# Kernel tuning notes

Measured on AMD Instinct MI355X. Metric: run time of the kernel, lower is better.

The kernel has to match this reference:

```python
import jax, jax.numpy as jnp
import numpy as np

N = 100000   # nodes
E = 1600000  # edges per meta-path graph
D_IN = 256
H = 4        # num_heads
F = 32       # out_feats per head
D_HID = H * F  # 128
D_SEM = 128  # semantic attention hidden dim
C = 8        # output classes
NEG_SLOPE = 0.2


def setup_inputs() -> dict:
    key = jax.random.key(0)
    ks = jax.random.split(key, 24)
    inp = {
        "x": jax.random.normal(ks[0], (N, D_IN), dtype=jnp.float32),
        "src0": jax.random.randint(ks[1], (E,), 0, N),
        "dst0": jax.random.randint(ks[2], (E,), 0, N),
        "ew0": jax.random.uniform(ks[3], (E,), dtype=jnp.float32),
        "src1": jax.random.randint(ks[4], (E,), 0, N),
        "dst1": jax.random.randint(ks[5], (E,), 0, N),
        "ew1": jax.random.uniform(ks[6], (E,), dtype=jnp.float32),
    }
    s_in = 1.0 / np.sqrt(D_IN)
    s_f = 1.0 / np.sqrt(F)
    s_h = 1.0 / np.sqrt(D_HID)
    s_s = 1.0 / np.sqrt(D_SEM)
    # GAT params for meta-path 0 and 1 (tuple feat -> separate fc_src/fc_dst)
    inp["Wsrc0"] = jax.random.normal(ks[7], (D_IN, D_HID), dtype=jnp.float32) * s_in
    inp["Wdst0"] = jax.random.normal(ks[8], (D_IN, D_HID), dtype=jnp.float32) * s_in
    inp["al0"] = jax.random.normal(ks[9], (H, F), dtype=jnp.float32) * s_f
    inp["ar0"] = jax.random.normal(ks[10], (H, F), dtype=jnp.float32) * s_f
    inp["b0"] = jnp.zeros((D_HID,), dtype=jnp.float32)
    inp["Wsrc1"] = jax.random.normal(ks[11], (D_IN, D_HID), dtype=jnp.float32) * s_in
    inp["Wdst1"] = jax.random.normal(ks[12], (D_IN, D_HID), dtype=jnp.float32) * s_in
    inp["al1"] = jax.random.normal(ks[13], (H, F), dtype=jnp.float32) * s_f
    inp["ar1"] = jax.random.normal(ks[14], (H, F), dtype=jnp.float32) * s_f
    inp["b1"] = jnp.zeros((D_HID,), dtype=jnp.float32)
    # Semantic attention: Linear(D_HID->128) -> tanh -> Linear(128->1, no bias)
    inp["Wp1"] = jax.random.normal(ks[15], (D_HID, D_SEM), dtype=jnp.float32) * s_h
    inp["bp1"] = jnp.zeros((D_SEM,), dtype=jnp.float32)
    inp["Wp2"] = jax.random.normal(ks[16], (D_SEM, 1), dtype=jnp.float32) * s_s
    # Prediction head
    inp["Wo"] = jax.random.normal(ks[17], (D_HID, C), dtype=jnp.float32) * s_h
    inp["bo"] = jnp.zeros((C,), dtype=jnp.float32)
    return inp


def gat_conv(x, Wsrc, Wdst, al, ar, b, src, dst, ew):
    # feat_src/feat_dst: [N, H, F]
    fs = (x @ Wsrc).reshape(N, H, F)
    fd = (x @ Wdst).reshape(N, H, F)
    el = jnp.einsum('nhf,hf->nh', fs, al)  # [N, H]
    er = jnp.einsum('nhf,hf->nh', fd, ar)  # [N, H]
    e = jax.nn.leaky_relu(el[src] + er[dst], negative_slope=NEG_SLOPE)  # [E, H]
    a = jax.nn.sigmoid(e) * ew[:, None]  # [E, H]  (sigmoid attention * edge_weight)
    m = fs[src] * a[:, :, None]  # [E, H, F]
    out = jax.ops.segment_sum(m, dst, num_segments=N)  # [N, H, F]
    out = out + b.reshape(1, H, F)
    return jax.nn.elu(out).reshape(N, H * F)


def semantic_attention(z, Wp1, bp1, Wp2):
    # z: [N, P, D_HID]
    w = jnp.tanh(z @ Wp1 + bp1) @ Wp2  # [N, P, 1]
    w = w.mean(axis=0)                  # [P, 1]
    beta = jax.nn.softmax(w, axis=0)    # softmax over meta-paths
    return (beta[None] * z).sum(axis=1)  # [N, D_HID]


def reference(x, src0, dst0, ew0, src1, dst1, ew1,
              Wsrc0, Wdst0, al0, ar0, b0,
              Wsrc1, Wdst1, al1, ar1, b1,
              Wp1, bp1, Wp2, Wo, bo):
    z0 = gat_conv(x, Wsrc0, Wdst0, al0, ar0, b0, src0, dst0, ew0)
    z1 = gat_conv(x, Wsrc1, Wdst1, al1, ar1, b1, src1, dst1, ew1)
    z = jnp.stack([z0, z1], axis=1)  # [N, 2, H*F]
    h = semantic_attention(z, Wp1, bp1, Wp2)  # [N, H*F]
    return h @ Wo + bo  # [N, C]
```

## Files before the change

### kernel.cpp

```cpp
#include <hip/hip_runtime.h>
#include <hip/hip_fp16.h>
#include <math.h>

#define N_NODES 100000
#define N_EDGES 1600000
#define D_IN    256
#define D_HID   128
#define NH      4
#define NF      32
#define D_SEM   128
#define NC      8
#define NEG_SLOPE 0.2f
#define BUCKET  64
#define BIN_SHIFT 9
#define BINS    196
#define BIN_CAP 9216
#define CHUNK   8192

typedef _Float16 half8 __attribute__((ext_vector_type(8)));
typedef float    floatx4 __attribute__((ext_vector_type(4)));

__global__ void prep_fold(const float* __restrict__ Ws0, const float* __restrict__ al0,
                          const float* __restrict__ Wd0, const float* __restrict__ ar0,
                          const float* __restrict__ Ws1, const float* __restrict__ al1,
                          const float* __restrict__ Wd1, const float* __restrict__ ar1,
                          float* __restrict__ WF) {
    int d = threadIdx.x;
    for (int p = 0; p < 2; ++p) {
        const float* Ws = p ? Ws1 : Ws0;
        const float* al = p ? al1 : al0;
        const float* Wd = p ? Wd1 : Wd0;
        const float* ar = p ? ar1 : ar0;
        for (int h = 0; h < NH; ++h) {
            float se = 0.f, sr = 0.f;
            for (int f = 0; f < NF; ++f) {
                se = fmaf(Ws[d*D_HID + h*NF + f], al[h*NF + f], se);
                sr = fmaf(Wd[d*D_HID + h*NF + f], ar[h*NF + f], sr);
            }
            WF[d*16 + p*8 + h]     = se;
            WF[d*16 + p*8 + 4 + h] = sr;
        }
    }
}

__global__ __launch_bounds__(256) void prep_tr(const float* __restrict__ Ws0,
                                               const float* __restrict__ Ws1,
                                               const float* __restrict__ Wp1,
                                               __half* __restrict__ WT0,
                                               __half* __restrict__ WT1,
                                               __half* __restrict__ WP1T) {
    int g = blockIdx.x * 256 + threadIdx.x;
    if (g < 32768) {
        int c = g >> 8, k = g & 255;
        WT0[g] = __float2half_rn(Ws0[k*D_HID + c]);
    } else if (g < 65536) {
        int g2 = g - 32768;
        int c = g2 >> 8, k = g2 & 255;
        WT1[g2] = __float2half_rn(Ws1[k*D_HID + c]);
    } else {
        int g2 = g - 65536;
        int c = g2 >> 7, k = g2 & 127;
        WP1T[g2] = __float2half_rn(Wp1[k*D_SEM + c]);
    }
}

__global__ __launch_bounds__(256) void er_el_kernel(const float* __restrict__ x,
                                                    const float* __restrict__ WF,
                                                    float* __restrict__ eler,
                                                    __half* __restrict__ XH) {
    __shared__ float xs[16][260];
    __shared__ float wfs[4096];
    int tid = threadIdx.x;
    #pragma unroll
    for (int i = 0; i < 16; ++i) wfs[tid + i*256] = WF[tid + i*256];
    int n0 = blockIdx.x * 16;
    #pragma unroll
    for (int i = 0; i < 4; ++i) {
        int id = tid + i*256;
        int r = id >> 6, c = (id & 63) << 2;
        *(float4*)&xs[r][c] = *(const float4*)&x[(size_t)(n0 + r)*D_IN + c];
    }
    __syncthreads();
    int node = tid >> 4, c = tid & 15;
    float s = 0.f;
    #pragma unroll 8
    for (int k = 0; k < 256; ++k) s = fmaf(xs[node][k], wfs[k*16 + c], s);
    int p = c >> 3, e = (c >> 2) & 1, h = c & 3;
    eler[(p*2 + e)*400000 + (n0 + node)*4 + h] = s;

    #pragma unroll
    for (int i = 0; i < 4; ++i) {
        int id = tid + i*256;
        int r = id >> 6, c4 = (id & 63) << 2;
        float4 v = *(const float4*)&xs[r][c4];
        __half2 h0 = __floats2half2_rn(v.x, v.y);
        __half2 h1 = __floats2half2_rn(v.z, v.w);
        uint2 pk; pk.x = *(unsigned*)&h0; pk.y = *(unsigned*)&h1;
        *(uint2*)&XH[(size_t)(n0 + r)*D_IN + c4] = pk;
    }
}

__global__ __launch_bounds__(256) void gemm_fs_mfma(const __half* __restrict__ XH,
                                                    const __half* __restrict__ WT,
                                                    __half* __restrict__ FS) {
    __shared__ unsigned short xs[64][64];
    __shared__ unsigned short ws[128][64];
    int tid = threadIdx.x;
    int row0 = blockIdx.x * 64;
    int wid = tid >> 6, lane = tid & 63;
    int wm = wid >> 1, wn = wid & 1;
    int lr = lane & 15, lk = lane >> 4;

    floatx4 acc[2][4];
    #pragma unroll
    for (int m = 0; m < 2; ++m)
        #pragma unroll
        for (int n = 0; n < 4; ++n) acc[m][n] = (floatx4){0.f, 0.f, 0.f, 0.f};

    for (int k0 = 0; k0 < D_IN; k0 += 64) {
        #pragma unroll
        for (int i = 0; i < 2; ++i) {
            int id = tid + i*256;
            int r = id >> 3, c8 = (id & 7) << 3;
            int grow = row0 + r;
            uint4 pk = make_uint4(0u, 0u, 0u, 0u);
            if (grow < N_NODES) pk = *(const uint4*)&XH[(size_t)grow*D_IN + k0 + c8];
            int cc = (((c8 >> 3) ^ (r & 7)) << 3);
            *(uint4*)&xs[r][cc] = pk;
        }
        #pragma unroll
        for (int i = 0; i < 8; ++i) {
            int id = tid + i*256;
            int col = id >> 4, c4 = (id & 15) << 2;
            uint2 pk = *(const uint2*)&WT[col*256 + k0 + c4];
            int cc = (((c4 >> 3) ^ (col & 7)) << 3) + (c4 & 7);
            *(uint2*)&ws[col][cc] = pk;
        }
        __syncthreads();
        #pragma unroll
        for (int kk = 0; kk < 2; ++kk) {
            int ksub = kk*4 + lk;
            half8 a[2], b[4];
            #pragma unroll
            for (int m = 0; m < 2; ++m) {
                int r = wm*32 + m*16 + lr;
                a[m] = *(half8*)&xs[r][((ksub ^ (r & 7)) << 3)];
            }
            #pragma unroll
            for (int n = 0; n < 4; ++n) {
                int c = wn*64 + n*16 + lr;
                b[n] = *(half8*)&ws[c][((ksub ^ (c & 7)) << 3)];
            }
            #pragma unroll
            for (int m = 0; m < 2; ++m)
                #pragma unroll
                for (int n = 0; n < 4; ++n)
                    acc[m][n] = __builtin_amdgcn_mfma_f32_16x16x32_f16(a[m], b[n], acc[m][n], 0, 0, 0);
        }
        __syncthreads();
    }

    unsigned short* outs = &ws[0][0];
    #pragma unroll
    for (int m = 0; m < 2; ++m)
        #pragma unroll
        for (int n = 0; n < 4; ++n) {
            int col = wn*64 + n*16 + lr;
            #pragma unroll
            for (int r4 = 0; r4 < 4; ++r4) {
                int rr = wm*32 + m*16 + lk*4 + r4;
                __half hv = __float2half_rn(acc[m][n][r4]);
                outs[rr*128 + col] = *(unsigned short*)&hv;
            }
        }
    __syncthreads();
    #pragma unroll
    for (int i = 0; i < 8; ++i) {
        int id = tid + i*256;
        int r = id >> 5, c4 = (id & 31) << 2;
        int grow = row0 + r;
        if (grow < N_NODES)
            *(uint2*)&FS[(size_t)grow*D_HID + c4] = *(uint2*)&outs[r*128 + c4];
    }
}

__global__ __launch_bounds__(1024) void bin_kernel(const int* __restrict__ src,
                                                   const int* __restrict__ dst,
                                                   const float* __restrict__ ew,
                                                   int* __restrict__ gcur,
                                                   uint2* __restrict__ binned) {
    __shared__ uint2 stage[CHUNK];
    __shared__ unsigned char binof[CHUNK];
    __shared__ int bcnt[256], boff[256], gbase[256], brun[256];
    int tid = threadIdx.x;
    int c0 = blockIdx.x * CHUNK;
    int C = N_EDGES - c0; if (C > CHUNK) C = CHUNK;
    if (C <= 0) return;

    if (tid < 256) bcnt[tid] = 0;
    __syncthreads();
    for (int j = tid; j < C; j += 1024)
        atomicAdd(&bcnt[dst[c0 + j] >> BIN_SHIFT], 1);
    __syncthreads();

    int v = (tid < 256) ? bcnt[tid] : 0;
    if (tid < 256) boff[tid] = v;
    __syncthreads();
    for (int o = 1; o < 256; o <<= 1) {
        int u = (tid < 256 && tid >= o) ? boff[tid - o] : 0;
        __syncthreads();
        if (tid < 256) boff[tid] += u;
        __syncthreads();
    }
    if (tid < 256) {
        boff[tid] -= v;
        brun[tid] = 0;
        if (tid < BINS) gbase[tid] = v ? atomicAdd(&gcur[tid], v) : 0;
    }
    __syncthreads();

    for (int j = tid; j < C; j += 1024) {
        int e = c0 + j;
        int d = dst[e];
        int b = d >> BIN_SHIFT;
        unsigned q = (unsigned)(ew[e] * 32767.f + 0.5f);
        int p = atomicAdd(&brun[b], 1);
        int sl = boff[b] + p;
        stage[sl] = make_uint2(((unsigned)src[e] << 15) | q, (unsigned)d);
        binof[sl] = (unsigned char)b;
    }
    __syncthreads();

    for (int j = tid; j < C; j += 1024) {
        int b = binof[j];
        int off = gbase[b] + (j - boff[b]);
        if (off < BIN_CAP) binned[b * BIN_CAP + off] = stage[j];
    }
}

__global__ __launch_bounds__(1024) void bucket_kernel(const int* __restrict__ gcur,
                                                      const uint2* __restrict__ binned,
                                                      int* __restrict__ cnt,
                                                      unsigned* __restrict__ edg) {
    __shared__ unsigned buck[512 * BUCKET];
    __shared__ int lcnt[512];
    int tid = threadIdx.x;
    int b = blockIdx.x;
    int n0 = b << BIN_SHIFT;
    if (tid < 512) lcnt[tid] = 0;
    __syncthreads();

    int cE = gcur[b]; if (cE > BIN_CAP) cE = BIN_CAP;
    for (int j = tid; j < cE; j += 1024) {
        uint2 r = binned[b * BIN_CAP + j];
        int dl = (int)r.y - n0;
        int p = atomicAdd(&lcnt[dl], 1);
        if (p < BUCKET) buck[(dl << 6) + p] = r.x;
    }
    __syncthreads();

    const uint4* b4 = (const uint4*)buck;
    uint4* e4 = (uint4*)edg;
    for (int i = tid; i < 512 * BUCKET / 4; i += 1024) {
        int node = n0 + (i >> 4);
        int used = lcnt[i >> 4];
        if (node < N_NODES && ((i & 15) << 2) < used)
            e4[((size_t)node << 4) + (i & 15)] = b4[i];
    }
    if (tid < 512) {
        int node = n0 + tid;
        if (node < N_NODES) cnt[node] = lcnt[tid] < BUCKET ? lcnt[tid] : BUCKET;
    }
}

__global__ __launch_bounds__(256) void agg_kernel(const __half* __restrict__ FS,
                                                  const float* __restrict__ el,
                                                  const float* __restrict__ er,
                                                  const int* __restrict__ cnt,
                                                  const unsigned* __restrict__ edg,
                                                  const float* __restrict__ bias,
                                                  float* __restrict__ z) {
    int wv = (blockIdx.x * 256 + threadIdx.x) >> 6;
    int lane = threadIdx.x & 63;
    if (wv >= N_NODES) return;
    int q  = lane >> 4;
    int ql = lane & 15;
    int h  = ql >> 2;
    float erh = er[wv*4 + h];
    int cn = cnt[wv];
    if (cn > BUCKET) cn = BUCKET;
    int beg = wv << 6;
    const __half* fsq = FS + (ql << 3);

    float4 a0 = make_float4(0.f,0.f,0.f,0.f);
    float4 a1 = make_float4(0.f,0.f,0.f,0.f);

    int j = q;
    for (; j + 4 < cn; j += 8) {
        unsigned p0 = edg[beg + j];
        unsigned p1 = edg[beg + j + 4];
        int s0 = p0 >> 15, s1 = p1 >> 15;
        uint4 raw0 = *(const uint4*)&fsq[s0*D_HID];
        uint4 raw1 = *(const uint4*)&fsq[s1*D_HID];
        float v0 = el[s0*4 + h] + erh;
        float v1 = el[s1*4 + h] + erh;
        float w0 = (float)(p0 & 32767u) * (1.f / 32767.f);
        float w1 = (float)(p1 & 32767u) * (1.f / 32767.f);
        v0 = v0 > 0.f ? v0 : NEG_SLOPE * v0;
        v1 = v1 > 0.f ? v1 : NEG_SLOPE * v1;
        float ac0 = w0 * __builtin_amdgcn_rcpf(1.f + __expf(-v0));
        float ac1 = w1 * __builtin_amdgcn_rcpf(1.f + __expf(-v1));
        float2 f0 = __half22float2(*(__half2*)&raw0.x);
        float2 f1 = __half22float2(*(__half2*)&raw0.y);
        float2 f2 = __half22float2(*(__half2*)&raw0.z);
        float2 f3 = __half22float2(*(__half2*)&raw0.w);
        a0.x = fmaf(f0.x, ac0, a0.x); a0.y = fmaf(f0.y, ac0, a0.y);
        a0.z = fmaf(f1.x, ac0, a0.z); a0.w = fmaf(f1.y, ac0, a0.w);
        a1.x = fmaf(f2.x, ac0, a1.x); a1.y = fmaf(f2.y, ac0, a1.y);
        a1.z = fmaf(f3.x, ac0, a1.z); a1.w = fmaf(f3.y, ac0, a1.w);
        f0 = __half22float2(*(__half2*)&raw1.x);
        f1 = __half22float2(*(__half2*)&raw1.y);
        f2 = __half22float2(*(__half2*)&raw1.z);
        f3 = __half22float2(*(__half2*)&raw1.w);
        a0.x = fmaf(f0.x, ac1, a0.x); a0.y = fmaf(f0.y, ac1, a0.y);
        a0.z = fmaf(f1.x, ac1, a0.z); a0.w = fmaf(f1.y, ac1, a0.w);
        a1.x = fmaf(f2.x, ac1, a1.x); a1.y = fmaf(f2.y, ac1, a1.y);
        a1.z = fmaf(f3.x, ac1, a1.z); a1.w = fmaf(f3.y, ac1, a1.w);
    }
    if (j < cn) {
        unsigned p = edg[beg + j];
        int s = p >> 15;
        float w = (float)(p & 32767u) * (1.f / 32767.f);
        float v = el[s*4 + h] + erh;
        v = v > 0.f ? v : NEG_SLOPE * v;
        float a = w * __builtin_amdgcn_rcpf(1.f + __expf(-v));
        uint4 raw = *(const uint4*)&fsq[s*D_HID];
        float2 f0 = __half22float2(*(__half2*)&raw.x);
        float2 f1 = __half22float2(*(__half2*)&raw.y);
        float2 f2 = __half22float2(*(__half2*)&raw.z);
        float2 f3 = __half22float2(*(__half2*)&raw.w);
        a0.x = fmaf(f0.x, a, a0.x); a0.y = fmaf(f0.y, a, a0.y);
        a0.z = fmaf(f1.x, a, a0.z); a0.w = fmaf(f1.y, a, a0.w);
        a1.x = fmaf(f2.x, a, a1.x); a1.y = fmaf(f2.y, a, a1.y);
        a1.z = fmaf(f3.x, a, a1.z); a1.w = fmaf(f3.y, a, a1.w);
    }

    #pragma unroll
    for (int o = 16; o < 64; o <<= 1) {
        a0.x += __shfl_xor(a0.x, o); a0.y += __shfl_xor(a0.y, o);
        a0.z += __shfl_xor(a0.z, o); a0.w += __shfl_xor(a0.w, o);
        a1.x += __shfl_xor(a1.x, o); a1.y += __shfl_xor(a1.y, o);
        a1.z += __shfl_xor(a1.z, o); a1.w += __shfl_xor(a1.w, o);
    }

    if (q < 2) {
        int c = (ql << 3) + (q << 2);
        float4 r = q ? a1 : a0;
        float4 bv = *(const float4*)&bias[c];
        r.x += bv.x; r.y += bv.y; r.z += bv.z; r.w += bv.w;
        r.x = r.x > 0.f ? r.x : expm1f(r.x);
        r.y = r.y > 0.f ? r.y : expm1f(r.y);
        r.z = r.z > 0.f ? r.z : expm1f(r.z);
        r.w = r.w > 0.f ? r.w : expm1f(r.w);
        *(float4*)&z[wv*D_HID + c] = r;
    }
}

__global__ __launch_bounds__(256) void sem_mfma(const float* __restrict__ z0,
                                                const float* __restrict__ z1,
                                                const __half* __restrict__ WP1T,
                                                const float* __restrict__ bp1,
                                                const float* __restrict__ Wp2,
                                                float* __restrict__ wsum) {
    __shared__ unsigned short zs[64][128];
    __shared__ unsigned short ps[128][128];
    __shared__ float red[4];
    const float* z = blockIdx.y ? z1 : z0;
    int tid = threadIdx.x;
    int row0 = blockIdx.x * 64;
    int wid = tid >> 6, lane = tid & 63;
    int wm = wid >> 1, wn = wid & 1;
    int lr = lane & 15, lk = lane >> 4;

    #pragma unroll
    for (int i = 0; i < 8; ++i) {
        int id = tid + i*256;
        int r = id >> 5, c4 = (id & 31) << 2;
        int grow = row0 + r;
        float4 v = make_float4(0.f, 0.f, 0.f, 0.f);
        if (grow < N_NODES) v = *(const float4*)&z[(size_t)grow*D_HID + c4];
        __half2 p0 = __floats2half2_rn(v.x, v.y);
        __half2 p1 = __floats2half2_rn(v.z, v.w);
        uint2 pk; pk.x = *(unsigned*)&p0; pk.y = *(unsigned*)&p1;
        int cc = (((c4 >> 3) ^ (r & 7)) << 3) + (c4 & 7);
        *(uint2*)&zs[r][cc] = pk;
    }
    #pragma unroll
    for (int i = 0; i < 16; ++i) {
        int id = tid + i*256;
        int c = id >> 5, k4 = (id & 31) << 2;
        uint2 pk = *(const uint2*)&WP1T[c*128 + k4];
        int cc = (((k4 >> 3) ^ (c & 7)) << 3) + (k4 & 7);
        *(uint2*)&ps[c][cc] = pk;
    }
    __syncthreads();

    floatx4 acc[2][4];
    #pragma unroll
    for (int m = 0; m < 2; ++m)
        #pragma unroll
        for (int n = 0; n < 4; ++n) acc[m][n] = (floatx4){0.f, 0.f, 0.f, 0.f};

    #pragma unroll
    for (int kk = 0; kk < 4; ++kk) {
        int ksub = kk*4 + lk;
        half8 a[2], b[4];
        #pragma unroll
        for (int m = 0; m < 2; ++m) {
            int r = wm*32 + m*16 + lr;
            a[m] = *(half8*)&zs[r][((ksub ^ (r & 7)) << 3)];
        }
        #pragma unroll
        for (int n = 0; n < 4; ++n) {
            int c = wn*64 + n*16 + lr;
            b[n] = *(half8*)&ps[c][((ksub ^ (c & 7)) << 3)];
        }
        #pragma unroll
        for (int m = 0; m < 2; ++m)
            #pragma unroll
            for (int n = 0; n < 4; ++n)
                acc[m][n] = __builtin_amdgcn_mfma_f32_16x16x32_f16(a[m], b[n], acc[m][n], 0, 0, 0);
    }

    float s = 0.f;
    #pragma unroll
    for (int m = 0; m < 2; ++m)
        #pragma unroll
        for (int n = 0; n < 4; ++n) {
            int col = wn*64 + n*16 + lr;
            float bp = bp1[col];
            float w2 = Wp2[col];
            #pragma unroll
            for (int r4 = 0; r4 < 4; ++r4) {
                int grow = row0 + wm*32 + m*16 + lk*4 + r4;
                if (grow < N_NODES) {
                    float v = acc[m][n][r4] + bp;
                    float t = 1.f - 2.f / (__expf(2.f*v) + 1.f);
                    s = fmaf(t, w2, s);
                }
            }
        }
    #pragma unroll
    for (int o = 1; o < 64; o <<= 1) s += __shfl_xor(s, o);
    if (lane == 0) red[wid] = s;
    __syncthreads();
    if (tid == 0) atomicAdd(&wsum[blockIdx.y], red[0] + red[1] + red[2] + red[3]);
}

__global__ __launch_bounds__(256) void final_kernel(const float* __restrict__ z0,
                                                    const float* __restrict__ z1,
                                                    const float* __restrict__ Wo,
                                                    const float* __restrict__ bo,
                                                    const float* __restrict__ wsum,
                                                    float* __restrict__ out) {
    __shared__ float z0s[32][132];
    __shared__ float z1s[32][132];
    __shared__ float wos[128*8];
    __shared__ float bos[8];
    int tid = threadIdx.x;
    int n0 = blockIdx.x * 32;
    #pragma unroll
    for (int i = 0; i < 4; ++i) wos[tid + i*256] = Wo[tid + i*256];
    if (tid < 8) bos[tid] = bo[tid];
    #pragma unroll
    for (int i = 0; i < 4; ++i) {
        int idx = tid + i*256;
        int r = idx >> 5, c = (idx & 31) << 2;
        *(float4*)&z0s[r][c] = *(const float4*)&z0[(n0 + r)*D_HID + c];
        *(float4*)&z1s[r][c] = *(const float4*)&z1[(n0 + r)*D_HID + c];
    }
    __syncthreads();

    float w0 = wsum[0] * (1.f / N_NODES), w1 = wsum[1] * (1.f / N_NODES);
    float m = fmaxf(w0, w1);
    float e0 = __expf(w0 - m), e1 = __expf(w1 - m);
    float b0 = e0 / (e0 + e1), b1 = 1.f - b0;

    int node = tid >> 3, c = tid & 7;
    float s = bos[c];
    #pragma unroll 8
    for (int k = 0; k < 128; ++k) {
        float hk = b0 * z0s[node][k] + b1 * z1s[node][k];
        s = fmaf(hk, wos[k*8 + c], s);
    }
    out[(n0 + node)*NC + c] = s;
}

extern "C" void kernel_launch(void* const* d_in, const int* in_sizes, int n_in,
                              void* d_out, int out_size, void* d_ws, size_t ws_size,
                              hipStream_t stream) {
    const float* x     = (const float*)d_in[0];
    const int*   src0  = (const int*)  d_in[1];
    const int*   dst0  = (const int*)  d_in[2];
    const float* ew0   = (const float*)d_in[3];
    const int*   src1  = (const int*)  d_in[4];
    const int*   dst1  = (const int*)  d_in[5];
    const float* ew1   = (const float*)d_in[6];
    const float* Wsrc0 = (const float*)d_in[7];
    const float* Wdst0 = (const float*)d_in[8];
    const float* al0   = (const float*)d_in[9];
    const float* ar0   = (const float*)d_in[10];
    const float* b0    = (const float*)d_in[11];
    const float* Wsrc1 = (const float*)d_in[12];
    const float* Wdst1 = (const float*)d_in[13];
    const float* al1   = (const float*)d_in[14];
    const float* ar1   = (const float*)d_in[15];
    const float* b1    = (const float*)d_in[16];
    const float* Wp1   = (const float*)d_in[17];
    const float* bp1   = (const float*)d_in[18];
    const float* Wp2   = (const float*)d_in[19];
    const float* Wo    = (const float*)d_in[20];
    const float* bo    = (const float*)d_in[21];
    float* out = (float*)d_out;

    float*    ws     = (float*)d_ws;
    __half*   FS     = (__half*)ws;
    float*    Z0     = ws    + 6400000;
    float*    Z1     = Z0    + 12800000;
    float*    ELER   = Z1    + 12800000;
    float*    WF     = ELER  + 1600000;
    float*    WSUM   = WF    + 4096;
    __half*   WT0    = (__half*)(WSUM + 8);
    __half*   WT1    = (__half*)((float*)WT0 + 16384);
    __half*   WP1T   = (__half*)((float*)WT1 + 16384);
    int*      CNT0   = (int*)((float*)WP1T + 8192);
    int*      CNT1   = CNT0  + 100000;
    int*      GCUR0  = CNT1  + 100000;
    int*      GCUR1  = GCUR0 + 256;
    unsigned* EDG    = (unsigned*)(GCUR1 + 256);
    uint2*    BINNED = (uint2*)(EDG + 6400000);
    __half*   XH     = (__half*)Z1;

    hipMemsetAsync(GCUR0, 0, sizeof(int)*512, stream);
    hipMemsetAsync(WSUM, 0, sizeof(float)*4, stream);

    prep_fold<<<1, 256, 0, stream>>>(Wsrc0, al0, Wdst0, ar0, Wsrc1, al1, Wdst1, ar1, WF);
    prep_tr<<<320, 256, 0, stream>>>(Wsrc0, Wsrc1, Wp1, WT0, WT1, WP1T);
    er_el_kernel<<<N_NODES/16, 256, 0, stream>>>(x, WF, ELER, XH);

    bin_kernel<<<BINS, 1024, 0, stream>>>(src0, dst0, ew0, GCUR0, BINNED);
    bucket_kernel<<<BINS, 1024, 0, stream>>>(GCUR0, BINNED, CNT0, EDG);
    gemm_fs_mfma<<<(N_NODES + 63)/64, 256, 0, stream>>>(XH, WT0, FS);
    agg_kernel<<<(N_NODES*64)/256, 256, 0, stream>>>(FS, ELER, ELER + 400000, CNT0, EDG, b0, Z0);

    bin_kernel<<<BINS, 1024, 0, stream>>>(src1, dst1, ew1, GCUR1, BINNED);
    bucket_kernel<<<BINS, 1024, 0, stream>>>(GCUR1, BINNED, CNT1, EDG);
    gemm_fs_mfma<<<(N_NODES + 63)/64, 256, 0, stream>>>(XH, WT1, FS);
    agg_kernel<<<(N_NODES*64)/256, 256, 0, stream>>>(FS, ELER + 800000, ELER + 1200000, CNT1, EDG, b1, Z1);

    dim3 semgrid((N_NODES + 63)/64, 2);
    sem_mfma<<<semgrid, 256, 0, stream>>>(Z0, Z1, WP1T, bp1, Wp2, WSUM);
    final_kernel<<<N_NODES/32, 256, 0, stream>>>(Z0, Z1, Wo, bo, WSUM, out);
}
```

Before: 616.9 us.

## Store GAT outputs in fp16 and dedupe per-edge attention across lanes

The aggregation kernel now writes its per-node outputs as fp16 instead of fp32. The semantic-attention and final kernels read the half-width data directly, which roughly halves that intermediate traffic and drops a conversion pass in sem_mfma. The edge loop is also restructured so that each lane computes one (edge, head) attention coefficient for 16 edges at a time. Source indices and coefficients are then shuffled to the lanes that gather features, instead of every lane recomputing the sigmoid redundantly. This costs fp16 rounding on the intermediate features and adds shuffle overhead, plus masked loads in partial tiles.

```diff
diff --git a/kernel.cpp b/kernel.cpp
--- a/kernel.cpp
+++ b/kernel.cpp
@@ -279,14 +279,14 @@
                                                   const int* __restrict__ cnt,
                                                   const unsigned* __restrict__ edg,
                                                   const float* __restrict__ bias,
-                                                  float* __restrict__ z) {
+                                                  __half* __restrict__ zh) {
     int wv = (blockIdx.x * 256 + threadIdx.x) >> 6;
     int lane = threadIdx.x & 63;
     if (wv >= N_NODES) return;
     int q  = lane >> 4;
     int ql = lane & 15;
-    int h  = ql >> 2;
-    float erh = er[wv*4 + h];
+    int hh = lane & 3;
+    float erh = er[wv*4 + hh];
     int cn = cnt[wv];
     if (cn > BUCKET) cn = BUCKET;
     int beg = wv << 6;
@@ -295,54 +295,35 @@
     float4 a0 = make_float4(0.f,0.f,0.f,0.f);
     float4 a1 = make_float4(0.f,0.f,0.f,0.f);
 
-    int j = q;
-    for (; j + 4 < cn; j += 8) {
-        unsigned p0 = edg[beg + j];
-        unsigned p1 = edg[beg + j + 4];
-        int s0 = p0 >> 15, s1 = p1 >> 15;
-        uint4 raw0 = *(const uint4*)&fsq[s0*D_HID];
-        uint4 raw1 = *(const uint4*)&fsq[s1*D_HID];
-        float v0 = el[s0*4 + h] + erh;
-        float v1 = el[s1*4 + h] + erh;
-        float w0 = (float)(p0 & 32767u) * (1.f / 32767.f);
-        float w1 = (float)(p1 & 32767u) * (1.f / 32767.f);
-        v0 = v0 > 0.f ? v0 : NEG_SLOPE * v0;
-        v1 = v1 > 0.f ? v1 : NEG_SLOPE * v1;
-        float ac0 = w0 * __builtin_amdgcn_rcpf(1.f + __expf(-v0));
-        float ac1 = w1 * __builtin_amdgcn_rcpf(1.f + __expf(-v1));
-        float2 f0 = __half22float2(*(__half2*)&raw0.x);
-        float2 f1 = __half22float2(*(__half2*)&raw0.y);
-        float2 f2 = __half22float2(*(__half2*)&raw0.z);
-        float2 f3 = __half22float2(*(__half2*)&raw0.w);
-        a0.x = fmaf(f0.x, ac0, a0.x); a0.y = fmaf(f0.y, ac0, a0.y);
-        a0.z = fmaf(f1.x, ac0, a0.z); a0.w = fmaf(f1.y, ac0, a0.w);
-        a1.x = fmaf(f2.x, ac0, a1.x); a1.y = fmaf(f2.y, ac0, a1.y);
-        a1.z = fmaf(f3.x, ac0, a1.z); a1.w = fmaf(f3.y, ac0, a1.w);
-        f0 = __half22float2(*(__half2*)&raw1.x);
-        f1 = __half22float2(*(__half2*)&raw1.y);
-        f2 = __half22float2(*(__half2*)&raw1.z);
-        f3 = __half22float2(*(__half2*)&raw1.w);
-        a0.x = fmaf(f0.x, ac1, a0.x); a0.y = fmaf(f0.y, ac1, a0.y);
-        a0.z = fmaf(f1.x, ac1, a0.z); a0.w = fmaf(f1.y, ac1, a0.w);
-        a1.x = fmaf(f2.x, ac1, a1.x); a1.y = fmaf(f2.y, ac1, a1.y);
-        a1.z = fmaf(f3.x, ac1, a1.z); a1.w = fmaf(f3.y, ac1, a1.w);
-    }
-    if (j < cn) {
-        unsigned p = edg[beg + j];
-        int s = p >> 15;
-        float w = (float)(p & 32767u) * (1.f / 32767.f);
-        float v = el[s*4 + h] + erh;
+    int nIt = (cn + 15) >> 4;
+    for (int it = 0; it < nIt; ++it) {
+        int jb = it << 4;
+        int sl = jb + (lane >> 2);
+        int slc = sl < cn ? sl : cn - 1;
+        unsigned w = edg[beg + slc];
+        int s = (int)(w >> 15);
+        float a = (float)(w & 32767u) * (1.f / 32767.f);
+        float v = el[s*4 + hh] + erh;
         v = v > 0.f ? v : NEG_SLOPE * v;
-        float a = w * __builtin_amdgcn_rcpf(1.f + __expf(-v));
-        uint4 raw = *(const uint4*)&fsq[s*D_HID];
-        float2 f0 = __half22float2(*(__half2*)&raw.x);
-        float2 f1 = __half22float2(*(__half2*)&raw.y);
-        float2 f2 = __half22float2(*(__half2*)&raw.z);
-        float2 f3 = __half22float2(*(__half2*)&raw.w);
-        a0.x = fmaf(f0.x, a, a0.x); a0.y = fmaf(f0.y, a, a0.y);
-        a0.z = fmaf(f1.x, a, a0.z); a0.w = fmaf(f1.y, a, a0.w);
-        a1.x = fmaf(f2.x, a, a1.x); a1.y = fmaf(f2.y, a, a1.y);
-        a1.z = fmaf(f3.x, a, a1.z); a1.w = fmaf(f3.y, a, a1.w);
+        a = a * __builtin_amdgcn_rcpf(1.f + __expf(-v));
+        a = sl < cn ? a : 0.f;
+        #pragma unroll
+        for (int u = 0; u < 4; ++u) {
+            int e = (u << 2) + q;
+            int su = jb + e;
+            int ssrc = __shfl(s, e << 2);
+            uint4 raw = make_uint4(0u, 0u, 0u, 0u);
+            if (su < cn) raw = *(const uint4*)&fsq[(size_t)ssrc * D_HID];
+            float av = __shfl(a, (e << 2) | (ql >> 2));
+            float2 f0 = __half22float2(*(__half2*)&raw.x);
+            float2 f1 = __half22float2(*(__half2*)&raw.y);
+            float2 f2 = __half22float2(*(__half2*)&raw.z);
+            float2 f3 = __half22float2(*(__half2*)&raw.w);
+            a0.x = fmaf(f0.x, av, a0.x); a0.y = fmaf(f0.y, av, a0.y);
+            a0.z = fmaf(f1.x, av, a0.z); a0.w = fmaf(f1.y, av, a0.w);
+            a1.x = fmaf(f2.x, av, a1.x); a1.y = fmaf(f2.y, av, a1.y);
+            a1.z = fmaf(f3.x, av, a1.z); a1.w = fmaf(f3.y, av, a1.w);
+        }
     }
 
     #pragma unroll
@@ -362,12 +343,15 @@
         r.y = r.y > 0.f ? r.y : expm1f(r.y);
         r.z = r.z > 0.f ? r.z : expm1f(r.z);
         r.w = r.w > 0.f ? r.w : expm1f(r.w);
-        *(float4*)&z[wv*D_HID + c] = r;
-    }
-}
-
-__global__ __launch_bounds__(256) void sem_mfma(const float* __restrict__ z0,
-                                                const float* __restrict__ z1,
+        __half2 h0 = __floats2half2_rn(r.x, r.y);
+        __half2 h1 = __floats2half2_rn(r.z, r.w);
+        uint2 pk; pk.x = *(unsigned*)&h0; pk.y = *(unsigned*)&h1;
+        *(uint2*)&zh[(size_t)wv*D_HID + c] = pk;
+    }
+}
+
+__global__ __launch_bounds__(256) void sem_mfma(const __half* __restrict__ zh0,
+                                                const __half* __restrict__ zh1,
                                                 const __half* __restrict__ WP1T,
                                                 const float* __restrict__ bp1,
                                                 const float* __restrict__ Wp2,
@@ -375,7 +359,7 @@
     __shared__ unsigned short zs[64][128];
     __shared__ unsigned short ps[128][128];
     __shared__ float red[4];
-    const float* z = blockIdx.y ? z1 : z0;
+    const __half* z = blockIdx.y ? zh1 : zh0;
     int tid = threadIdx.x;
     int row0 = blockIdx.x * 64;
     int wid = tid >> 6, lane = tid & 63;
@@ -383,17 +367,13 @@
     int lr = lane & 15, lk = lane >> 4;
 
     #pragma unroll
-    for (int i = 0; i < 8; ++i) {
+    for (int i = 0; i < 4; ++i) {
         int id = tid + i*256;
-        int r = id >> 5, c4 = (id & 31) << 2;
+        int r = id >> 4, ch = id & 15;
         int grow = row0 + r;
-        float4 v = make_float4(0.f, 0.f, 0.f, 0.f);
-        if (grow < N_NODES) v = *(const float4*)&z[(size_t)grow*D_HID + c4];
-        __half2 p0 = __floats2half2_rn(v.x, v.y);
-        __half2 p1 = __floats2half2_rn(v.z, v.w);
-        uint2 pk; pk.x = *(unsigned*)&p0; pk.y = *(unsigned*)&p1;
-        int cc = (((c4 >> 3) ^ (r & 7)) << 3) + (c4 & 7);
-        *(uint2*)&zs[r][cc] = pk;
+        uint4 pk = make_uint4(0u, 0u, 0u, 0u);
+        if (grow < N_NODES) pk = *(const uint4*)&z[(size_t)grow*D_HID + (ch << 3)];
+        *(uint4*)&zs[r][((ch ^ (r & 7)) << 3)] = pk;
     }
     #pragma unroll
     for (int i = 0; i < 16; ++i) {
@@ -457,8 +437,8 @@
     if (tid == 0) atomicAdd(&wsum[blockIdx.y], red[0] + red[1] + red[2] + red[3]);
 }
 
-__global__ __launch_bounds__(256) void final_kernel(const float* __restrict__ z0,
-                                                    const float* __restrict__ z1,
+__global__ __launch_bounds__(256) void final_kernel(const __half* __restrict__ zh0,
+                                                    const __half* __restrict__ zh1,
                                                     const float* __restrict__ Wo,
                                                     const float* __restrict__ bo,
                                                     const float* __restrict__ wsum,
@@ -473,11 +453,23 @@
     for (int i = 0; i < 4; ++i) wos[tid + i*256] = Wo[tid + i*256];
     if (tid < 8) bos[tid] = bo[tid];
     #pragma unroll
-    for (int i = 0; i < 4; ++i) {
-        int idx = tid + i*256;
-        int r = idx >> 5, c = (idx & 31) << 2;
-        *(float4*)&z0s[r][c] = *(const float4*)&z0[(n0 + r)*D_HID + c];
-        *(float4*)&z1s[r][c] = *(const float4*)&z1[(n0 + r)*D_HID + c];
+    for (int i = 0; i < 2; ++i) {
+        int id = tid + i*256;
+        int r = id >> 4, c8 = (id & 15) << 3;
+        uint4 p0 = *(const uint4*)&zh0[(size_t)(n0 + r)*D_HID + c8];
+        uint4 p1 = *(const uint4*)&zh1[(size_t)(n0 + r)*D_HID + c8];
+        float2 q0 = __half22float2(*(__half2*)&p0.x);
+        float2 q1 = __half22float2(*(__half2*)&p0.y);
+        float2 q2 = __half22float2(*(__half2*)&p0.z);
+        float2 q3 = __half22float2(*(__half2*)&p0.w);
+        *(float4*)&z0s[r][c8]     = make_float4(q0.x, q0.y, q1.x, q1.y);
+        *(float4*)&z0s[r][c8 + 4] = make_float4(q2.x, q2.y, q3.x, q3.y);
+        q0 = __half22float2(*(__half2*)&p1.x);
+        q1 = __half22float2(*(__half2*)&p1.y);
+        q2 = __half22float2(*(__half2*)&p1.z);
+        q3 = __half22float2(*(__half2*)&p1.w);
+        *(float4*)&z1s[r][c8]     = make_float4(q0.x, q0.y, q1.x, q1.y);
+        *(float4*)&z1s[r][c8 + 4] = make_float4(q2.x, q2.y, q3.x, q3.y);
     }
     __syncthreads();
 
@@ -525,11 +517,12 @@
 
     float*    ws     = (float*)d_ws;
     __half*   FS     = (__half*)ws;
-    float*    Z0     = ws    + 6400000;
-    float*    Z1     = Z0    + 12800000;
-    float*    ELER   = Z1    + 12800000;
-    float*    WF     = ELER  + 1600000;
-    float*    WSUM   = WF    + 4096;
+    __half*   ZH0    = (__half*)(ws + 6400000);
+    __half*   ZH1    = (__half*)(ws + 12800000);
+    __half*   XH     = (__half*)(ws + 19200000);
+    float*    ELER   = ws + 32000000;
+    float*    WF     = ELER + 1600000;
+    float*    WSUM   = WF + 4096;
     __half*   WT0    = (__half*)(WSUM + 8);
     __half*   WT1    = (__half*)((float*)WT0 + 16384);
     __half*   WP1T   = (__half*)((float*)WT1 + 16384);
@@ -539,7 +532,6 @@
     int*      GCUR1  = GCUR0 + 256;
     unsigned* EDG    = (unsigned*)(GCUR1 + 256);
     uint2*    BINNED = (uint2*)(EDG + 6400000);
-    __half*   XH     = (__half*)Z1;
 
     hipMemsetAsync(GCUR0, 0, sizeof(int)*512, stream);
     hipMemsetAsync(WSUM, 0, sizeof(float)*4, stream);
@@ -551,14 +543,14 @@
     bin_kernel<<<BINS, 1024, 0, stream>>>(src0, dst0, ew0, GCUR0, BINNED);
     bucket_kernel<<<BINS, 1024, 0, stream>>>(GCUR0, BINNED, CNT0, EDG);
     gemm_fs_mfma<<<(N_NODES + 63)/64, 256, 0, stream>>>(XH, WT0, FS);
-    agg_kernel<<<(N_NODES*64)/256, 256, 0, stream>>>(FS, ELER, ELER + 400000, CNT0, EDG, b0, Z0);
+    agg_kernel<<<(N_NODES*64)/256, 256, 0, stream>>>(FS, ELER, ELER + 400000, CNT0, EDG, b0, ZH0);
 
     bin_kernel<<<BINS, 1024, 0, stream>>>(src1, dst1, ew1, GCUR1, BINNED);
     bucket_kernel<<<BINS, 1024, 0, stream>>>(GCUR1, BINNED, CNT1, EDG);
     gemm_fs_mfma<<<(N_NODES + 63)/64, 256, 0, stream>>>(XH, WT1, FS);
-    agg_kernel<<<(N_NODES*64)/256, 256, 0, stream>>>(FS, ELER + 800000, ELER + 1200000, CNT1, EDG, b1, Z1);
+    agg_kernel<<<(N_NODES*64)/256, 256, 0, stream>>>(FS, ELER + 800000, ELER + 1200000, CNT1, EDG, b1, ZH1);
 
     dim3 semgrid((N_NODES + 63)/64, 2);
-    sem_mfma<<<semgrid, 256, 0, stream>>>(Z0, Z1, WP1T, bp1, Wp2, WSUM);
-    final_kernel<<<N_NODES/32, 256, 0, stream>>>(Z0, Z1, Wo, bo, WSUM, out);
-}
+    sem_mfma<<<semgrid, 256, 0, stream>>>(ZH0, ZH1, WP1T, bp1, Wp2, WSUM);
+    final_kernel<<<N_NODES/32, 256, 0, stream>>>(ZH0, ZH1, Wo, bo, WSUM, out);
+}
```

Result: faster. 599.8 us (-2.8%).
